# Optimization experiments

Measured on AMD Instinct MI355X. Metric: run time of the kernel, lower is better.

Reference implementation:

```python
import jax, jax.numpy as jnp
import numpy as np

EMBED_DIM = 1024
NUM_HEADS = 16
HEAD_DIM = EMBED_DIM // NUM_HEADS


def setup_inputs() -> dict:
    key = jax.random.key(0)
    ks = jax.random.split(key, 9)
    B, T, C = 2, 2048, EMBED_DIM
    s = 1.0 / np.sqrt(C)
    return {
        "x": jax.random.normal(ks[0], (B, T, C), dtype=jnp.float32),
        "Wq": jax.random.normal(ks[1], (C, C), dtype=jnp.float32) * s,
        "bq": jnp.zeros((C,), dtype=jnp.float32),
        "Wk": jax.random.normal(ks[2], (C, C), dtype=jnp.float32) * s,
        "bk": jnp.zeros((C,), dtype=jnp.float32),
        "Wv": jax.random.normal(ks[3], (C, C), dtype=jnp.float32) * s,
        "bv": jnp.zeros((C,), dtype=jnp.float32),
        "Wo": jax.random.normal(ks[4], (C, C), dtype=jnp.float32) * s,
        "bo": jnp.zeros((C,), dtype=jnp.float32),
    }


def reference(x, Wq, bq, Wk, bk, Wv, bv, Wo, bo):
    B, T, C = x.shape
    H, D = NUM_HEADS, HEAD_DIM
    # projections (torch Linear: x @ W.T + b; here W stored as [in,out])
    q = (x @ Wq + bq).reshape(B, T, H, D).transpose(0, 2, 1, 3)  # [B,H,T,D]
    k = (x @ Wk + bk).reshape(B, T, H, D).transpose(0, 2, 1, 3)
    v = (x @ Wv + bv).reshape(B, T, H, D).transpose(0, 2, 1, 3)
    scores = jnp.einsum("bhtd,bhsd->bhts", q, k) / jnp.sqrt(jnp.float32(D))
    causal = jnp.tril(jnp.ones((T, T), dtype=bool))  # keep lower triangle
    scores = jnp.where(causal, scores, -jnp.inf)
    weights = jax.nn.softmax(scores, axis=-1)
    attended = jnp.einsum("bhts,bhsd->bhtd", weights, v)
    attended = attended.transpose(0, 2, 1, 3).reshape(B, T, C)
    return attended @ Wo + bo
```

## Files before the change

kernel.cpp:

```cpp
#include <hip/hip_runtime.h>
#include <math.h>


#define BLOCK 256

typedef __attribute__((ext_vector_type(8))) short bf16x8;
typedef __attribute__((ext_vector_type(4))) float f32x4;

__device__ inline short f2bf(float f) {
  union { float f; unsigned u; } c; c.f = f;
  unsigned u = c.u;
  unsigned r = (u + 0x7fffu + ((u >> 16) & 1u)) >> 16;
  return (short)r;
}

#define GLD_LDS16(g, l)                                            \
  __builtin_amdgcn_global_load_lds(                                \
      (const __attribute__((address_space(1))) unsigned int*)(g),  \
      (__attribute__((address_space(3))) unsigned int*)(l), 16, 0, 0)


__global__ void cvt_x_kernel(const float* __restrict__ x, short* __restrict__ xb) {
  int i = (blockIdx.x * BLOCK + threadIdx.x) * 8;
  float4 a = *(const float4*)(x + i);
  float4 b = *(const float4*)(x + i + 4);
  alignas(16) short o[8];
  o[0] = f2bf(a.x); o[1] = f2bf(a.y); o[2] = f2bf(a.z); o[3] = f2bf(a.w);
  o[4] = f2bf(b.x); o[5] = f2bf(b.y); o[6] = f2bf(b.z); o[7] = f2bf(b.w);
  *(int4*)(xb + i) = *(int4*)o;
}

__global__ void cvt_w_kernel(const float* __restrict__ Wq, const float* __restrict__ Wk,
                             const float* __restrict__ Wv, const float* __restrict__ Wo,
                             short* __restrict__ Wtqkv, short* __restrict__ Wto) {
  __shared__ float tile[32][33];
  int z = blockIdx.z;
  const float* W = (z == 0) ? Wq : (z == 1) ? Wk : (z == 2) ? Wv : Wo;
  short* outp = (z == 3) ? Wto : (Wtqkv + (size_t)z * 1024 * 1024);
  int k0 = blockIdx.x * 32, n0 = blockIdx.y * 32;
  int tr = threadIdx.x >> 5, tc = threadIdx.x & 31;
#pragma unroll
  for (int i = 0; i < 4; i++)
    tile[tr + i * 8][tc] = W[(k0 + tr + i * 8) * 1024 + n0 + tc];
  __syncthreads();
#pragma unroll
  for (int i = 0; i < 4; i++)
    outp[(n0 + tr + i * 8) * 1024 + k0 + tc] = f2bf(tile[tc][tr + i * 8]);
}


__global__ __launch_bounds__(BLOCK) void gemm_qkv_kernel(
    const short* __restrict__ A, const short* __restrict__ Wt,
    const float* __restrict__ bq, const float* __restrict__ bk,
    const float* __restrict__ bv,
    short* __restrict__ Qo, short* __restrict__ Ko, short* __restrict__ Vo) {
  const int Kd = 1024;
  const float QSCL = 0.18033688011f;
  int m0 = blockIdx.x * 128, n0 = blockIdx.y * 128;
  int t = threadIdx.x;
  int lane = t & 63, wv = t >> 6;
  int quad = lane >> 4, lc = lane & 15;
  int wy = wv >> 1, wx = wv & 1;
  __shared__ short As[128 * 32];
  __shared__ short Bs[128 * 32];
  int r0 = t >> 2, c0 = (t & 3) * 8;
  f32x4 acc[4][4] = {};
  const short* Arow0 = A + (size_t)(m0 + r0) * Kd + c0;
  const short* Arow1 = A + (size_t)(m0 + r0 + 64) * Kd + c0;
  const short* Brow0 = Wt + (size_t)(n0 + r0) * Kd + c0;
  const short* Brow1 = Wt + (size_t)(n0 + r0 + 64) * Kd + c0;
  for (int k0 = 0; k0 < Kd; k0 += 32) {
    __syncthreads();
    GLD_LDS16(Arow0 + k0, &As[8 * t]);
    GLD_LDS16(Arow1 + k0, &As[8 * t + 2048]);
    GLD_LDS16(Brow0 + k0, &Bs[8 * t]);
    GLD_LDS16(Brow1 + k0, &Bs[8 * t + 2048]);
    __syncthreads();
    bf16x8 af[4], bf[4];
#pragma unroll
    for (int i = 0; i < 4; i++)
      af[i] = *(const bf16x8*)&As[(wy * 64 + i * 16 + lc) * 32 + quad * 8];
#pragma unroll
    for (int i = 0; i < 4; i++)
      bf[i] = *(const bf16x8*)&Bs[(wx * 64 + i * 16 + lc) * 32 + quad * 8];
#pragma unroll
    for (int mi = 0; mi < 4; mi++)
#pragma unroll
      for (int ni = 0; ni < 4; ni++)
        acc[mi][ni] = __builtin_amdgcn_mfma_f32_16x16x32_bf16(af[mi], bf[ni], acc[mi][ni], 0, 0, 0);
  }
#pragma unroll
  for (int mi = 0; mi < 4; mi++) {
    int row = m0 + wy * 64 + mi * 16 + quad * 4;
#pragma unroll
    for (int ni = 0; ni < 4; ni++) {
      int col = n0 + wx * 64 + ni * 16 + lc;
      int which = col >> 10;
      int hd = col & 1023;
      int h = hd >> 6, d = hd & 63;
      float bb = (which == 0) ? bq[hd] : (which == 1) ? bk[hd] : bv[hd];
#pragma unroll
      for (int r = 0; r < 4; r++) {
        int rw = row + r;
        int b = rw >> 11, tt = rw & 2047;
        float val = acc[mi][ni][r] + bb;
        if (which == 0) {
          Qo[((size_t)(b * 16 + h) * 2048 + tt) * 64 + d] = f2bf(val * QSCL);
        } else if (which == 1) {
          Ko[((size_t)(b * 16 + h) * 2048 + tt) * 64 + d] = f2bf(val);
        } else {
          int tl = tt & 63;
          int tt2 = (tt & ~63) | ((tl & 15) * 4 + (tl >> 4));
          Vo[((size_t)(b * 16 + h) * 64 + d) * 2048 + tt2] = f2bf(val);
        }
      }
    }
  }
}


__global__ __launch_bounds__(BLOCK) void gemm_out_kernel(
    const short* __restrict__ A, const short* __restrict__ Wt,
    const float* __restrict__ bias, float* __restrict__ Out) {
  const int Kd = 1024;
  int m0 = blockIdx.x * 128, n0 = blockIdx.y * 128;
  int t = threadIdx.x;
  int lane = t & 63, wv = t >> 6;
  int quad = lane >> 4, lc = lane & 15;
  int wy = wv >> 1, wx = wv & 1;
  __shared__ short As[128 * 32];
  __shared__ short Bs[128 * 32];
  int r0 = t >> 2, c0 = (t & 3) * 8;
  f32x4 acc[4][4] = {};
  const short* Arow0 = A + (size_t)(m0 + r0) * Kd + c0;
  const short* Arow1 = A + (size_t)(m0 + r0 + 64) * Kd + c0;
  const short* Brow0 = Wt + (size_t)(n0 + r0) * Kd + c0;
  const short* Brow1 = Wt + (size_t)(n0 + r0 + 64) * Kd + c0;
  for (int k0 = 0; k0 < Kd; k0 += 32) {
    __syncthreads();
    GLD_LDS16(Arow0 + k0, &As[8 * t]);
    GLD_LDS16(Arow1 + k0, &As[8 * t + 2048]);
    GLD_LDS16(Brow0 + k0, &Bs[8 * t]);
    GLD_LDS16(Brow1 + k0, &Bs[8 * t + 2048]);
    __syncthreads();
    bf16x8 af[4], bf[4];
#pragma unroll
    for (int i = 0; i < 4; i++)
      af[i] = *(const bf16x8*)&As[(wy * 64 + i * 16 + lc) * 32 + quad * 8];
#pragma unroll
    for (int i = 0; i < 4; i++)
      bf[i] = *(const bf16x8*)&Bs[(wx * 64 + i * 16 + lc) * 32 + quad * 8];
#pragma unroll
    for (int mi = 0; mi < 4; mi++)
#pragma unroll
      for (int ni = 0; ni < 4; ni++)
        acc[mi][ni] = __builtin_amdgcn_mfma_f32_16x16x32_bf16(af[mi], bf[ni], acc[mi][ni], 0, 0, 0);
  }
#pragma unroll
  for (int mi = 0; mi < 4; mi++) {
    int row = m0 + wy * 64 + mi * 16 + quad * 4;
#pragma unroll
    for (int ni = 0; ni < 4; ni++) {
      int col = n0 + wx * 64 + ni * 16 + lc;
      float bb = bias[col];
#pragma unroll
      for (int r = 0; r < 4; r++)
        Out[(size_t)(row + r) * 1024 + col] = acc[mi][ni][r] + bb;
    }
  }
}


__global__ __launch_bounds__(BLOCK) void attn_kernel(
    const short* __restrict__ Q, const short* __restrict__ K,
    const short* __restrict__ Vt, short* __restrict__ Oa) {
  int bh = blockIdx.x >> 4;
  int pair = blockIdx.x & 15;
  int t = threadIdx.x;
  int lane = t & 63, w = t >> 6;
  int quad = lane >> 4, lc = lane & 15;
  const short* Qb = Q + (size_t)bh * 2048 * 64;
  const short* Kb = K + (size_t)bh * 2048 * 64;
  const short* Vg = Vt + (size_t)bh * 64 * 2048;
  int b = bh >> 4, h = bh & 15;

  __shared__ short Kt[64 * 72];
  __shared__ short Vs[64 * 72];
  __shared__ short Ps[4][16 * 72];
  short* Pw = &Ps[w][0];

  int srow = t >> 2;
  int scol = (t & 3) * 16;
  const float M2 = 14.5f;

  bf16x8 ones;
#pragma unroll
  for (int e = 0; e < 8; e++) ones[e] = (short)0x3F80;

  for (int pass = 0; pass < 2; pass++) {
    int j = pass ? (31 - pair) : pair;
    int q0 = j * 64;
    bf16x8 qf[2];
    qf[0] = *(const bf16x8*)&Qb[(size_t)(q0 + w * 16 + lc) * 64 + quad * 8];
    qf[1] = *(const bf16x8*)&Qb[(size_t)(q0 + w * 16 + lc) * 64 + 32 + quad * 8];
    f32x4 oacc[4] = {};
    f32x4 lacc = {0.f, 0.f, 0.f, 0.f};

    int4 ka0 = *(const int4*)&Kb[(size_t)srow * 64 + scol];
    int4 ka1 = *(const int4*)&Kb[(size_t)srow * 64 + scol + 8];
    int4 va0 = *(const int4*)&Vg[(size_t)srow * 2048 + scol];
    int4 va1 = *(const int4*)&Vg[(size_t)srow * 2048 + scol + 8];
    __syncthreads();
    *(int4*)&Kt[srow * 72 + scol] = ka0;
    *(int4*)&Kt[srow * 72 + scol + 8] = ka1;
    *(int4*)&Vs[srow * 72 + scol] = va0;
    *(int4*)&Vs[srow * 72 + scol + 8] = va1;
    __syncthreads();

    for (int kt = 0; kt <= j; kt++) {
      if (kt < j) {
        int kbase = (kt + 1) * 64;
        ka0 = *(const int4*)&Kb[(size_t)(kbase + srow) * 64 + scol];
        ka1 = *(const int4*)&Kb[(size_t)(kbase + srow) * 64 + scol + 8];
        va0 = *(const int4*)&Vg[(size_t)srow * 2048 + kbase + scol];
        va1 = *(const int4*)&Vg[(size_t)srow * 2048 + kbase + scol + 8];
      }
      f32x4 s[4] = {};
#pragma unroll
      for (int ng = 0; ng < 4; ng++)
#pragma unroll
        for (int kf = 0; kf < 2; kf++) {
          bf16x8 kfr = *(const bf16x8*)&Kt[(ng * 16 + lc) * 72 + kf * 32 + quad * 8];
          s[ng] = __builtin_amdgcn_mfma_f32_16x16x32_bf16(qf[kf], kfr, s[ng], 0, 0, 0);
        }
      if (kt == j) {
        int rowl = w * 16 + quad * 4;
#pragma unroll
        for (int ng = 0; ng < 4; ng++) {
          int keyl = ng * 16 + lc;
#pragma unroll
          for (int r = 0; r < 4; r++)
            if (keyl > rowl + r) s[ng][r] = -3.0e38f;
        }
      }
#pragma unroll
      for (int r = 0; r < 4; r++) {
        unsigned u[4];
#pragma unroll
        for (int ng = 0; ng < 4; ng++) {
          union { float f; unsigned v; } cc;
          cc.f = __builtin_amdgcn_exp2f(s[ng][r] - M2);
          u[ng] = cc.v + 0x8000u;
        }
        int2 pk;
        pk.x = (int)__builtin_amdgcn_perm(u[1], u[0], 0x07060302);
        pk.y = (int)__builtin_amdgcn_perm(u[3], u[2], 0x07060302);
        *(int2*)&Pw[(quad * 4 + r) * 72 + 4 * lc] = pk;
      }
#pragma unroll
      for (int kf = 0; kf < 2; kf++) {
        bf16x8 pf = *(const bf16x8*)&Pw[lc * 72 + kf * 32 + quad * 8];
        lacc = __builtin_amdgcn_mfma_f32_16x16x32_bf16(pf, ones, lacc, 0, 0, 0);
#pragma unroll
        for (int nt = 0; nt < 4; nt++) {
          bf16x8 vf = *(const bf16x8*)&Vs[(nt * 16 + lc) * 72 + kf * 32 + quad * 8];
          oacc[nt] = __builtin_amdgcn_mfma_f32_16x16x32_bf16(pf, vf, oacc[nt], 0, 0, 0);
        }
      }
      if (kt < j) {
        __syncthreads();
        *(int4*)&Kt[srow * 72 + scol] = ka0;
        *(int4*)&Kt[srow * 72 + scol + 8] = ka1;
        *(int4*)&Vs[srow * 72 + scol] = va0;
        *(int4*)&Vs[srow * 72 + scol + 8] = va1;
        __syncthreads();
      }
    }

#pragma unroll
    for (int r = 0; r < 4; r++) {
      float inv = 1.0f / lacc[r];
      int tt = q0 + w * 16 + quad * 4 + r;
#pragma unroll
      for (int nt = 0; nt < 4; nt++)
        Oa[(size_t)(b * 2048 + tt) * 1024 + h * 64 + nt * 16 + lc] =
            f2bf(oacc[nt][r] * inv);
    }
  }
}


extern "C" void kernel_launch(void* const* d_in, const int* in_sizes, int n_in,
                              void* d_out, int out_size, void* d_ws, size_t ws_size,
                              hipStream_t stream) {
  const float* x = (const float*)d_in[0];
  const float* Wq = (const float*)d_in[1];
  const float* bq = (const float*)d_in[2];
  const float* Wk = (const float*)d_in[3];
  const float* bk = (const float*)d_in[4];
  const float* Wv = (const float*)d_in[5];
  const float* bv = (const float*)d_in[6];
  const float* Wo = (const float*)d_in[7];
  const float* bo = (const float*)d_in[8];
  char* ws = (char*)d_ws;
  const size_t MB = 1024 * 1024;
  short* xb = (short*)(ws);
  short* Wtqkv = (short*)(ws + 8 * MB);
  short* Wto = (short*)(ws + 14 * MB);
  short* Qb = (short*)(ws + 17 * MB);
  short* Kb = (short*)(ws + 25 * MB);
  short* Vb = (short*)(ws + 33 * MB);
  short* Att = (short*)(ws + 41 * MB);
  float* out = (float*)d_out;

  cvt_x_kernel<<<2048, BLOCK, 0, stream>>>(x, xb);
  cvt_w_kernel<<<dim3(32, 32, 4), BLOCK, 0, stream>>>(Wq, Wk, Wv, Wo, Wtqkv, Wto);
  gemm_qkv_kernel<<<dim3(32, 24), BLOCK, 0, stream>>>(xb, Wtqkv, bq, bk, bv, Qb, Kb, Vb);
  attn_kernel<<<512, BLOCK, 0, stream>>>(Qb, Kb, Vb, Att);
  gemm_out_kernel<<<dim3(32, 8), BLOCK, 0, stream>>>(Att, Wto, bo, out);
}
```

Baseline: 197.5 us.

## Restructure attention to 32x32 MFMA with split-K waves and direct global fragment loads

Rewrites the attention kernel to use 32x32x16 MFMA tiles with 2-wave blocks of 32 query rows. The two waves split the key tiles between them and combine their partial outputs and row sums through shared memory. K and V fragments are now loaded straight from global memory instead of staged through LDS with block barriers, and row sums are accumulated in registers rather than by an extra ones-MFMA. The V layout written by the QKV GEMM changes to plain transposed with packed 4-element stores, to match the new fragment loads. The aim is fewer barriers and more parallelism (1024 blocks), at the cost of redundant global loads, since each wave reads K/V independently, and no LDS reuse of K/V.

Result: slower. 235.2 us (+19.1%).

```diff
diff --git a/kernel.cpp b/kernel.cpp
--- a/kernel.cpp
+++ b/kernel.cpp
@@ -6,6 +6,7 @@
 
 typedef __attribute__((ext_vector_type(8))) short bf16x8;
 typedef __attribute__((ext_vector_type(4))) float f32x4;
+typedef __attribute__((ext_vector_type(16))) float f32x16;
 
 __device__ inline short f2bf(float f) {
   union { float f; unsigned u; } c; c.f = f;
@@ -99,19 +100,23 @@
       int hd = col & 1023;
       int h = hd >> 6, d = hd & 63;
       float bb = (which == 0) ? bq[hd] : (which == 1) ? bk[hd] : bv[hd];
-#pragma unroll
-      for (int r = 0; r < 4; r++) {
-        int rw = row + r;
-        int b = rw >> 11, tt = rw & 2047;
-        float val = acc[mi][ni][r] + bb;
-        if (which == 0) {
-          Qo[((size_t)(b * 16 + h) * 2048 + tt) * 64 + d] = f2bf(val * QSCL);
-        } else if (which == 1) {
-          Ko[((size_t)(b * 16 + h) * 2048 + tt) * 64 + d] = f2bf(val);
-        } else {
-          int tl = tt & 63;
-          int tt2 = (tt & ~63) | ((tl & 15) * 4 + (tl >> 4));
-          Vo[((size_t)(b * 16 + h) * 64 + d) * 2048 + tt2] = f2bf(val);
+      if (which == 2) {
+        alignas(8) short pk[4];
+#pragma unroll
+        for (int r = 0; r < 4; r++) pk[r] = f2bf(acc[mi][ni][r] + bb);
+        int b = row >> 11, tt = row & 2047;
+        *(int2*)&Vo[((size_t)(b * 16 + h) * 64 + d) * 2048 + tt] = *(const int2*)pk;
+      } else {
+#pragma unroll
+        for (int r = 0; r < 4; r++) {
+          int rw = row + r;
+          int b = rw >> 11, tt = rw & 2047;
+          float val = acc[mi][ni][r] + bb;
+          if (which == 0) {
+            Qo[((size_t)(b * 16 + h) * 2048 + tt) * 64 + d] = f2bf(val * QSCL);
+          } else {
+            Ko[((size_t)(b * 16 + h) * 2048 + tt) * 64 + d] = f2bf(val);
+          }
         }
       }
     }
@@ -171,121 +176,128 @@
 }
 
 
-__global__ __launch_bounds__(BLOCK) void attn_kernel(
+__global__ __launch_bounds__(128, 2) void attn_kernel(
     const short* __restrict__ Q, const short* __restrict__ K,
     const short* __restrict__ Vt, short* __restrict__ Oa) {
-  int bh = blockIdx.x >> 4;
-  int pair = blockIdx.x & 15;
+  int bh = blockIdx.x >> 5;
+  int pair = blockIdx.x & 31;
   int t = threadIdx.x;
   int lane = t & 63, w = t >> 6;
-  int quad = lane >> 4, lc = lane & 15;
+  int ln = lane & 31, lh = lane >> 5;
   const short* Qb = Q + (size_t)bh * 2048 * 64;
   const short* Kb = K + (size_t)bh * 2048 * 64;
   const short* Vg = Vt + (size_t)bh * 64 * 2048;
   int b = bh >> 4, h = bh & 15;
 
-  __shared__ short Kt[64 * 72];
-  __shared__ short Vs[64 * 72];
-  __shared__ short Ps[4][16 * 72];
-  short* Pw = &Ps[w][0];
-
-  int srow = t >> 2;
-  int scol = (t & 3) * 16;
+  __shared__ short Pbuf[2][32 * 72];
+  __shared__ float obuf[32][64];
+  __shared__ float lbuf[2][64];
+  short* Pw = Pbuf[w];
+
   const float M2 = 14.5f;
 
-  bf16x8 ones;
-#pragma unroll
-  for (int e = 0; e < 8; e++) ones[e] = (short)0x3F80;
-
-  for (int pass = 0; pass < 2; pass++) {
-    int j = pass ? (31 - pair) : pair;
-    int q0 = j * 64;
-    bf16x8 qf[2];
-    qf[0] = *(const bf16x8*)&Qb[(size_t)(q0 + w * 16 + lc) * 64 + quad * 8];
-    qf[1] = *(const bf16x8*)&Qb[(size_t)(q0 + w * 16 + lc) * 64 + 32 + quad * 8];
-    f32x4 oacc[4] = {};
-    f32x4 lacc = {0.f, 0.f, 0.f, 0.f};
-
-    int4 ka0 = *(const int4*)&Kb[(size_t)srow * 64 + scol];
-    int4 ka1 = *(const int4*)&Kb[(size_t)srow * 64 + scol + 8];
-    int4 va0 = *(const int4*)&Vg[(size_t)srow * 2048 + scol];
-    int4 va1 = *(const int4*)&Vg[(size_t)srow * 2048 + scol + 8];
-    __syncthreads();
-    *(int4*)&Kt[srow * 72 + scol] = ka0;
-    *(int4*)&Kt[srow * 72 + scol + 8] = ka1;
-    *(int4*)&Vs[srow * 72 + scol] = va0;
-    *(int4*)&Vs[srow * 72 + scol + 8] = va1;
-    __syncthreads();
-
-    for (int kt = 0; kt <= j; kt++) {
-      if (kt < j) {
-        int kbase = (kt + 1) * 64;
-        ka0 = *(const int4*)&Kb[(size_t)(kbase + srow) * 64 + scol];
-        ka1 = *(const int4*)&Kb[(size_t)(kbase + srow) * 64 + scol + 8];
-        va0 = *(const int4*)&Vg[(size_t)srow * 2048 + kbase + scol];
-        va1 = *(const int4*)&Vg[(size_t)srow * 2048 + kbase + scol + 8];
+  for (int sp = 0; sp < 2; sp++) {
+    int s = sp ? (63 - pair) : pair;
+    int q0 = s * 32;
+    bf16x8 qf[4];
+#pragma unroll
+    for (int c = 0; c < 4; c++)
+      qf[c] = *(const bf16x8*)&Qb[(size_t)(q0 + ln) * 64 + c * 16 + lh * 8];
+
+    f32x16 O0 = {}, O1 = {};
+    float lsum = 0.f;
+    int ntiles = (s >> 1) + 1;
+
+    for (int kt = w; kt < ntiles; kt += 2) {
+      int kbase = kt * 64;
+      bf16x8 kfr[2][4];
+#pragma unroll
+      for (int kh = 0; kh < 2; kh++)
+#pragma unroll
+        for (int c = 0; c < 4; c++)
+          kfr[kh][c] = *(const bf16x8*)&Kb[(size_t)(kbase + kh * 32 + ln) * 64 + c * 16 + lh * 8];
+      bf16x8 vfr[2][4];
+#pragma unroll
+      for (int dh = 0; dh < 2; dh++)
+#pragma unroll
+        for (int c = 0; c < 4; c++)
+          vfr[dh][c] = *(const bf16x8*)&Vg[(size_t)(dh * 32 + ln) * 2048 + kbase + c * 16 + lh * 8];
+
+      f32x16 S[2] = {};
+#pragma unroll
+      for (int kh = 0; kh < 2; kh++)
+#pragma unroll
+        for (int c = 0; c < 4; c++)
+          S[kh] = __builtin_amdgcn_mfma_f32_32x32x16_bf16(kfr[kh][c], qf[c], S[kh], 0, 0, 0);
+
+      if (kt == ntiles - 1) {
+        int qg = q0 + ln;
+#pragma unroll
+        for (int kh = 0; kh < 2; kh++)
+#pragma unroll
+          for (int reg = 0; reg < 16; reg++) {
+            int key = kbase + kh * 32 + (reg & 3) + 8 * (reg >> 2) + 4 * lh;
+            if (key > qg) S[kh][reg] = -3.0e38f;
+          }
       }
-      f32x4 s[4] = {};
-#pragma unroll
-      for (int ng = 0; ng < 4; ng++)
-#pragma unroll
-        for (int kf = 0; kf < 2; kf++) {
-          bf16x8 kfr = *(const bf16x8*)&Kt[(ng * 16 + lc) * 72 + kf * 32 + quad * 8];
-          s[ng] = __builtin_amdgcn_mfma_f32_16x16x32_bf16(qf[kf], kfr, s[ng], 0, 0, 0);
+
+#pragma unroll
+      for (int kh = 0; kh < 2; kh++)
+#pragma unroll
+        for (int g = 0; g < 4; g++) {
+          unsigned u[4];
+#pragma unroll
+          for (int i = 0; i < 4; i++) {
+            union { float f; unsigned v; } cc;
+            cc.f = __builtin_amdgcn_exp2f(S[kh][g * 4 + i] - M2);
+            lsum += cc.f;
+            u[i] = cc.v + 0x8000u;
+          }
+          int2 pk;
+          pk.x = (int)__builtin_amdgcn_perm(u[1], u[0], 0x07060302);
+          pk.y = (int)__builtin_amdgcn_perm(u[3], u[2], 0x07060302);
+          *(int2*)&Pw[ln * 72 + kh * 32 + g * 8 + lh * 4] = pk;
         }
-      if (kt == j) {
-        int rowl = w * 16 + quad * 4;
-#pragma unroll
-        for (int ng = 0; ng < 4; ng++) {
-          int keyl = ng * 16 + lc;
-#pragma unroll
-          for (int r = 0; r < 4; r++)
-            if (keyl > rowl + r) s[ng][r] = -3.0e38f;
+
+      bf16x8 pf[4];
+#pragma unroll
+      for (int c = 0; c < 4; c++)
+        pf[c] = *(const bf16x8*)&Pw[ln * 72 + c * 16 + lh * 8];
+
+#pragma unroll
+      for (int c = 0; c < 4; c++) {
+        O0 = __builtin_amdgcn_mfma_f32_32x32x16_bf16(vfr[0][c], pf[c], O0, 0, 0, 0);
+        O1 = __builtin_amdgcn_mfma_f32_32x32x16_bf16(vfr[1][c], pf[c], O1, 0, 0, 0);
+      }
+    }
+
+    lbuf[w][lane] = lsum;
+    if (w == 0) {
+#pragma unroll
+      for (int reg = 0; reg < 16; reg++) {
+        obuf[reg][lane] = O0[reg];
+        obuf[16 + reg][lane] = O1[reg];
+      }
+    }
+    __syncthreads();
+    if (w == 1) {
+      float lt = lbuf[0][ln] + lbuf[0][ln + 32] + lbuf[1][ln] + lbuf[1][ln + 32];
+      float inv = 1.0f / lt;
+      size_t rowbase = (size_t)(b * 2048 + q0 + ln) * 1024 + h * 64;
+#pragma unroll
+      for (int dh = 0; dh < 2; dh++)
+#pragma unroll
+        for (int g = 0; g < 4; g++) {
+          alignas(8) short pk[4];
+#pragma unroll
+          for (int i = 0; i < 4; i++) {
+            float v = (dh ? O1[g * 4 + i] : O0[g * 4 + i]) + obuf[dh * 16 + g * 4 + i][lane];
+            pk[i] = f2bf(v * inv);
+          }
+          *(int2*)&Oa[rowbase + dh * 32 + g * 8 + lh * 4] = *(const int2*)pk;
         }
-      }
-#pragma unroll
-      for (int r = 0; r < 4; r++) {
-        unsigned u[4];
-#pragma unroll
-        for (int ng = 0; ng < 4; ng++) {
-          union { float f; unsigned v; } cc;
-          cc.f = __builtin_amdgcn_exp2f(s[ng][r] - M2);
-          u[ng] = cc.v + 0x8000u;
-        }
-        int2 pk;
-        pk.x = (int)__builtin_amdgcn_perm(u[1], u[0], 0x07060302);
-        pk.y = (int)__builtin_amdgcn_perm(u[3], u[2], 0x07060302);
-        *(int2*)&Pw[(quad * 4 + r) * 72 + 4 * lc] = pk;
-      }
-#pragma unroll
-      for (int kf = 0; kf < 2; kf++) {
-        bf16x8 pf = *(const bf16x8*)&Pw[lc * 72 + kf * 32 + quad * 8];
-        lacc = __builtin_amdgcn_mfma_f32_16x16x32_bf16(pf, ones, lacc, 0, 0, 0);
-#pragma unroll
-        for (int nt = 0; nt < 4; nt++) {
-          bf16x8 vf = *(const bf16x8*)&Vs[(nt * 16 + lc) * 72 + kf * 32 + quad * 8];
-          oacc[nt] = __builtin_amdgcn_mfma_f32_16x16x32_bf16(pf, vf, oacc[nt], 0, 0, 0);
-        }
-      }
-      if (kt < j) {
-        __syncthreads();
-        *(int4*)&Kt[srow * 72 + scol] = ka0;
-        *(int4*)&Kt[srow * 72 + scol + 8] = ka1;
-        *(int4*)&Vs[srow * 72 + scol] = va0;
-        *(int4*)&Vs[srow * 72 + scol + 8] = va1;
-        __syncthreads();
-      }
-    }
-
-#pragma unroll
-    for (int r = 0; r < 4; r++) {
-      float inv = 1.0f / lacc[r];
-      int tt = q0 + w * 16 + quad * 4 + r;
-#pragma unroll
-      for (int nt = 0; nt < 4; nt++)
-        Oa[(size_t)(b * 2048 + tt) * 1024 + h * 64 + nt * 16 + lc] =
-            f2bf(oacc[nt][r] * inv);
-    }
+    }
+    __syncthreads();
   }
 }
 
@@ -316,6 +328,6 @@
   cvt_x_kernel<<<2048, BLOCK, 0, stream>>>(x, xb);
   cvt_w_kernel<<<dim3(32, 32, 4), BLOCK, 0, stream>>>(Wq, Wk, Wv, Wo, Wtqkv, Wto);
   gemm_qkv_kernel<<<dim3(32, 24), BLOCK, 0, stream>>>(xb, Wtqkv, bq, bk, bv, Qb, Kb, Vb);
-  attn_kernel<<<512, BLOCK, 0, stream>>>(Qb, Kb, Vb, Att);
+  attn_kernel<<<1024, 128, 0, stream>>>(Qb, Kb, Vb, Att);
   gemm_out_kernel<<<dim3(32, 8), BLOCK, 0, stream>>>(Att, Wto, bo, out);
 }
```
